# Optimization experiments

Measured on AMD Instinct MI355X. Metric: run time of the kernel, lower is better.

The kernel has to match this reference:

```python
import jax, jax.numpy as jnp
import numpy as np

D_MODEL = 1024
NHEAD = 16
HEAD_DIM = D_MODEL // NHEAD
DIM_FF = 4096
B, TC, TP = 4, 1024, 1024
EPS = 1e-5


def _layernorm(x, g, b):
    mu = jnp.mean(x, axis=-1, keepdims=True)
    var = jnp.mean(jnp.square(x - mu), axis=-1, keepdims=True)
    return (x - mu) * jax.lax.rsqrt(var + EPS) * g + b


def setup_inputs() -> dict:
    key = jax.random.key(0)
    ks = jax.random.split(key, 12)
    s = 0.02
    return {
        "x": jax.random.normal(ks[0], (B, TC, D_MODEL), jnp.float32),
        "Kp": jax.random.normal(ks[1], (B, NHEAD, TP, HEAD_DIM), jnp.float32),
        "Vp": jax.random.normal(ks[2], (B, NHEAD, TP, HEAD_DIM), jnp.float32),
        "pos_offset": TP,
        "wqkv": jax.random.normal(ks[3], (D_MODEL, 3 * D_MODEL), jnp.float32) * s,
        "bqkv": jnp.zeros((3 * D_MODEL,), jnp.float32),
        "wo": jax.random.normal(ks[4], (D_MODEL, D_MODEL), jnp.float32) * s,
        "bo": jnp.zeros((D_MODEL,), jnp.float32),
        "g1": jnp.ones((D_MODEL,), jnp.float32),
        "be1": jnp.zeros((D_MODEL,), jnp.float32),
        "g2": jnp.ones((D_MODEL,), jnp.float32),
        "be2": jnp.zeros((D_MODEL,), jnp.float32),
        "w1": jax.random.normal(ks[5], (D_MODEL, DIM_FF), jnp.float32) * s,
        "bf1": jnp.zeros((DIM_FF,), jnp.float32),
        "w2": jax.random.normal(ks[6], (DIM_FF, D_MODEL), jnp.float32) * s,
        "bf2": jnp.zeros((D_MODEL,), jnp.float32),
    }


def reference(x, Kp, Vp, pos_offset, wqkv, bqkv, wo, bo, g1, be1, g2, be2, w1, bf1, w2, bf2):
    Bsz, Tc, D = x.shape
    H, Dh = NHEAD, HEAD_DIM
    h = _layernorm(x, g1, be1)
    qkv = (h @ wqkv + bqkv).reshape(Bsz, Tc, 3, H, Dh).transpose(2, 0, 3, 1, 4)
    q, k_new, v_new = qkv[0], qkv[1], qkv[2]  # [B,H,Tc,Dh]
    K = jnp.concatenate([Kp, k_new], axis=2)  # [B,H,Tk,Dh]
    V = jnp.concatenate([Vp, v_new], axis=2)
    Tk = K.shape[2]
    scale = Dh ** -0.5
    # fused causal-masked attention; equivalent to the per-token loop:
    # query i attends keys j with j <= pos_offset + i
    scores = jnp.einsum("bhqd,bhkd->bhqk", q, K) * scale
    q_idx = jnp.arange(Tc)[:, None]
    k_idx = jnp.arange(Tk)[None, :]
    mask = k_idx <= (pos_offset + q_idx)  # [Tc,Tk]
    scores = jnp.where(mask, scores, jnp.finfo(scores.dtype).min)
    attn = jax.nn.softmax(scores, axis=-1)
    o = jnp.einsum("bhqk,bhkd->bhqd", attn, V)
    o = o.transpose(0, 2, 1, 3).reshape(Bsz, Tc, D)
    x = x + o @ wo + bo
    h2 = _layernorm(x, g2, be2)
    ff = jax.nn.gelu(h2 @ w1 + bf1, approximate=False) @ w2 + bf2
    x = x + ff
    return x, K, V
```

## Files before the change

### kernel.cpp

```cpp
#include <hip/hip_runtime.h>
#include <math.h>

#define DM   1024
#define NH   16
#define DH   64
#define DFF  4096
#define BSZ  4
#define TCC  1024
#define TPP  1024
#define TKK  2048
#define NTOK (BSZ*TCC)

typedef __attribute__((ext_vector_type(8))) short bf16x8;
typedef __attribute__((ext_vector_type(4))) float f32x4;

__device__ __forceinline__ unsigned short f2bf(float x) {
  union { float f; unsigned u; } v; v.f = x;
  unsigned r = v.u + 0x7fffu + ((v.u >> 16) & 1u);
  return (unsigned short)(r >> 16);
}
__device__ __forceinline__ unsigned pk2(float a, float b) {
  return (unsigned)f2bf(a) | ((unsigned)f2bf(b) << 16);
}

__device__ __forceinline__ void gload16(const void* g, void* l) {
  __builtin_amdgcn_global_load_lds(
      (const __attribute__((address_space(1))) void*)g,
      (__attribute__((address_space(3))) void*)l, 16, 0, 0);
}

__device__ __forceinline__ float wave_reduce_sum(float v) {
#pragma unroll
  for (int off = 32; off > 0; off >>= 1)
    v += __shfl_down(v, off, 64);
  return v;
}

__device__ __forceinline__ float gelu_f(float x) {
  return 0.5f * x * (1.0f + erff(x * 0.70710678118654752440f));
}

__global__ __launch_bounds__(256) void castT_kernel(
    const float* __restrict__ W, unsigned short* __restrict__ Wt, int K, int N) {
  __shared__ float tile[32][33];
  int nb = blockIdx.x << 5, kb = blockIdx.y << 5;
  int c = threadIdx.x & 31, r8 = threadIdx.x >> 5;
#pragma unroll
  for (int i = 0; i < 32; i += 8)
    tile[r8 + i][c] = W[(size_t)(kb + r8 + i) * N + nb + c];
  __syncthreads();
#pragma unroll
  for (int i = 0; i < 32; i += 8)
    Wt[(size_t)(nb + r8 + i) * K + kb + c] = f2bf(tile[c][r8 + i]);
}

__global__ __launch_bounds__(256) void castVt_kernel(
    const float* __restrict__ V, unsigned short* __restrict__ Vt) {
  __shared__ float tile[32][33];
  int z = blockIdx.z;
  const float* W = V + (size_t)z * TKK * DH;
  unsigned short* Wt = Vt + (size_t)z * DH * TKK;
  int nb = blockIdx.x << 5;
  int kb = blockIdx.y << 5;
  int c = threadIdx.x & 31, r8 = threadIdx.x >> 5;
#pragma unroll
  for (int i = 0; i < 32; i += 8)
    tile[r8 + i][c] = W[(size_t)(kb + r8 + i) * DH + nb + c];
  __syncthreads();
#pragma unroll
  for (int i = 0; i < 32; i += 8)
    Wt[(size_t)(nb + r8 + i) * TKK + kb + c] = f2bf(tile[c][r8 + i]);
}

__global__ __launch_bounds__(256) void copy_kv_kernel(
    const float4* __restrict__ Kp, const float4* __restrict__ Vp,
    float4* __restrict__ Kout, float4* __restrict__ Vout) {
  int idx = blockIdx.x * 256 + threadIdx.x;
  int r = idx >> 4;
  int c = idx & 15;
  int dr = (r >> 10) * TKK + (r & 1023);
  Kout[dr * 16 + c] = Kp[idx];
  Vout[dr * 16 + c] = Vp[idx];
}

__global__ __launch_bounds__(256) void ln_kernel(
    const float* __restrict__ x, const float* __restrict__ g,
    const float* __restrict__ b, unsigned short* __restrict__ out) {
  __shared__ float red[8];
  int row = blockIdx.x;
  int tid = threadIdx.x;
  const float4* xr = (const float4*)(x + (size_t)row * DM);
  float4 xv = xr[tid];
  float s  = xv.x + xv.y + xv.z + xv.w;
  float ss = xv.x*xv.x + xv.y*xv.y + xv.z*xv.z + xv.w*xv.w;
  s  = wave_reduce_sum(s);
  ss = wave_reduce_sum(ss);
  int lane = tid & 63, wid = tid >> 6;
  if (lane == 0) { red[wid] = s; red[4 + wid] = ss; }
  __syncthreads();
  s  = red[0] + red[1] + red[2] + red[3];
  ss = red[4] + red[5] + red[6] + red[7];
  float mu  = s * (1.0f / DM);
  float var = ss * (1.0f / DM) - mu * mu;
  float rs  = rsqrtf(var + 1e-5f);
  float4 gv = ((const float4*)g)[tid];
  float4 bv = ((const float4*)b)[tid];
  ushort4 ov;
  ov.x = f2bf((xv.x - mu) * rs * gv.x + bv.x);
  ov.y = f2bf((xv.y - mu) * rs * gv.y + bv.y);
  ov.z = f2bf((xv.z - mu) * rs * gv.z + bv.z);
  ov.w = f2bf((xv.w - mu) * rs * gv.w + bv.w);
  *(ushort4*)&out[(size_t)row * DM + tid * 4] = ov;
}

template <int MODE>
__global__ __launch_bounds__(256) void mm_kernel(
    const unsigned short* __restrict__ A, const unsigned short* __restrict__ Bt,
    const float* __restrict__ bias, const float* __restrict__ res,
    float* __restrict__ outf, unsigned short* __restrict__ outb,
    float* __restrict__ Kc, float* __restrict__ Vc,
    int M, int N, int K) {
  __shared__ __align__(16) short As[128 * 32];
  __shared__ __align__(16) short Bs[128 * 32];
  int tid = threadIdx.x;
  int w = tid >> 6, l = tid & 63;
  int m0 = blockIdx.y << 7, n0 = blockIdx.x << 7;
  int wm = (w >> 1) << 6, wn = (w & 1) << 6;
  int cidx = l & 15, rg = l >> 4;
  f32x4 acc[4][4] = {};

  int idx0 = w * 1024 + l * 16;
  int idx1 = idx0 + 4096;
  const char* gA0 = (const char*)A + (size_t)(m0 + (idx0 >> 6)) * 2 * K + (idx0 & 63);
  const char* gA1 = (const char*)A + (size_t)(m0 + (idx1 >> 6)) * 2 * K + (idx1 & 63);
  const char* gB0 = (const char*)Bt + (size_t)(n0 + (idx0 >> 6)) * 2 * K + (idx0 & 63);
  const char* gB1 = (const char*)Bt + (size_t)(n0 + (idx1 >> 6)) * 2 * K + (idx1 & 63);
  char* lA0 = (char*)As + idx0; char* lA1 = (char*)As + idx1;
  char* lB0 = (char*)Bs + idx0; char* lB1 = (char*)Bs + idx1;

  for (int k0 = 0; k0 < K; k0 += 32) {
    gload16(gA0, lA0); gload16(gA1, lA1);
    gload16(gB0, lB0); gload16(gB1, lB1);
    gA0 += 64; gA1 += 64; gB0 += 64; gB1 += 64;
    __syncthreads();
    bf16x8 af[4], bfr[4];
#pragma unroll
    for (int i = 0; i < 4; ++i) {
      af[i]  = *(const bf16x8*)&As[(wm + i * 16 + cidx) * 32 + rg * 8];
      bfr[i] = *(const bf16x8*)&Bs[(wn + i * 16 + cidx) * 32 + rg * 8];
    }
#pragma unroll
    for (int i = 0; i < 4; ++i)
#pragma unroll
      for (int j = 0; j < 4; ++j)
        acc[i][j] = __builtin_amdgcn_mfma_f32_16x16x32_bf16(
            af[i], bfr[j], acc[i][j], 0, 0, 0);
    __syncthreads();
  }

#pragma unroll
  for (int i = 0; i < 4; ++i) {
#pragma unroll
    for (int j = 0; j < 4; ++j) {
      int col = n0 + wn + j * 16 + cidx;
      float bb = bias[col];
#pragma unroll
      for (int r = 0; r < 4; ++r) {
        int row = m0 + wm + i * 16 + rg * 4 + r;
        float v = acc[i][j][r] + bb;
        if (MODE == 0) {
          int which = col >> 10, c = col & 1023;
          int hh = c >> 6, dd = c & 63;
          int b = row >> 10, t = row & 1023;
          size_t base = (size_t)(b * NH + hh);
          if (which == 0)      outb[(base * TCC + t) * DH + dd] = f2bf(v * 0.125f);
          else if (which == 1) Kc[(base * TKK + TPP + t) * DH + dd] = v;
          else                 Vc[(base * TKK + TPP + t) * DH + dd] = v;
        } else if (MODE == 1) {
          size_t off = (size_t)row * N + col;
          outf[off] = res[off] + v;
        } else {
          outb[(size_t)row * N + col] = f2bf(gelu_f(v));
        }
      }
    }
  }
}

__global__ __launch_bounds__(256) void attn_kernel(
    const unsigned short* __restrict__ Qb, const float* __restrict__ K,
    const unsigned short* __restrict__ Vtb, const int* __restrict__ posp,
    unsigned short* __restrict__ o) {
  __shared__ __align__(16) unsigned short Qs[64][72];
  __shared__ __align__(16) unsigned short Ks[64][72];
  __shared__ __align__(16) unsigned short Vts[64][72];
  __shared__ __align__(16) unsigned short Pw[4][16][72];
  int tid = threadIdx.x;
  int w = tid >> 6, lane = tid & 63;
  int l15 = lane & 15, quad = lane >> 4;
  int blk = blockIdx.x;
  int bh = blk >> 4;
  int qbase = (blk & 15) << 6;
  int b = bh >> 4, h = bh & 15;
  int pos = *posp;

  {
    int r = tid >> 2, cg = (tid & 3) << 4;
    const unsigned short* src = Qb + ((size_t)bh * TCC + qbase + r) * DH + cg;
    *(uint4*)&Qs[r][cg]     = *(const uint4*)src;
    *(uint4*)&Qs[r][cg + 8] = *(const uint4*)(src + 8);
  }
  __syncthreads();
  bf16x8 aq0 = *(const bf16x8*)&Qs[16 * w + l15][quad * 8];
  bf16x8 aq1 = *(const bf16x8*)&Qs[16 * w + l15][32 + quad * 8];

  f32x4 accO[4] = {};
  f32x4 accL = {};
  bf16x8 ones;
#pragma unroll
  for (int i = 0; i < 8; ++i) ones[i] = (short)0x3F80;

  int nk = pos + qbase + 64; if (nk > TKK) nk = TKK;
  int ntiles = nk >> 6;
  const float* Kbh = K + (size_t)bh * TKK * DH;
  const unsigned short* Vbh = Vtb + (size_t)bh * DH * TKK;

  for (int t = 0; t < ntiles; ++t) {
    int kt = t << 6;
    {
      int r = tid >> 2, cg = (tid & 3) << 4;
      const float* ks = Kbh + (size_t)(kt + r) * DH + cg;
      float4 k0 = *(const float4*)ks,       k1 = *(const float4*)(ks + 4);
      float4 k2 = *(const float4*)(ks + 8), k3 = *(const float4*)(ks + 12);
      uint4 p0, p1;
      p0.x = pk2(k0.x, k0.y); p0.y = pk2(k0.z, k0.w);
      p0.z = pk2(k1.x, k1.y); p0.w = pk2(k1.z, k1.w);
      p1.x = pk2(k2.x, k2.y); p1.y = pk2(k2.z, k2.w);
      p1.z = pk2(k3.x, k3.y); p1.w = pk2(k3.z, k3.w);
      *(uint4*)&Ks[r][cg]     = p0;
      *(uint4*)&Ks[r][cg + 8] = p1;
      const unsigned short* vs = Vbh + (size_t)r * TKK + kt + cg;
      *(uint4*)&Vts[r][cg]     = *(const uint4*)vs;
      *(uint4*)&Vts[r][cg + 8] = *(const uint4*)(vs + 8);
    }
    __syncthreads();
    f32x4 accS[4] = {};
#pragma unroll
    for (int j = 0; j < 4; ++j) {
      bf16x8 bk0 = *(const bf16x8*)&Ks[16 * j + l15][quad * 8];
      bf16x8 bk1 = *(const bf16x8*)&Ks[16 * j + l15][32 + quad * 8];
      accS[j] = __builtin_amdgcn_mfma_f32_16x16x32_bf16(aq0, bk0, accS[j], 0, 0, 0);
      accS[j] = __builtin_amdgcn_mfma_f32_16x16x32_bf16(aq1, bk1, accS[j], 0, 0, 0);
    }
    bool edge = (kt + 63 > pos + qbase);
#pragma unroll
    for (int j = 0; j < 4; ++j) {
      int key = kt + 16 * j + l15;
#pragma unroll
      for (int r = 0; r < 4; ++r) {
        float p = __expf(accS[j][r]);
        if (edge && key > pos + qbase + 16 * w + quad * 4 + r) p = 0.f;
        Pw[w][quad * 4 + r][16 * j + l15] = f2bf(p);
      }
    }
    bf16x8 ap0 = *(const bf16x8*)&Pw[w][l15][quad * 8];
    bf16x8 ap1 = *(const bf16x8*)&Pw[w][l15][32 + quad * 8];
    accL = __builtin_amdgcn_mfma_f32_16x16x32_bf16(ap0, ones, accL, 0, 0, 0);
    accL = __builtin_amdgcn_mfma_f32_16x16x32_bf16(ap1, ones, accL, 0, 0, 0);
#pragma unroll
    for (int j2 = 0; j2 < 4; ++j2) {
      bf16x8 bv0 = *(const bf16x8*)&Vts[16 * j2 + l15][quad * 8];
      bf16x8 bv1 = *(const bf16x8*)&Vts[16 * j2 + l15][32 + quad * 8];
      accO[j2] = __builtin_amdgcn_mfma_f32_16x16x32_bf16(ap0, bv0, accO[j2], 0, 0, 0);
      accO[j2] = __builtin_amdgcn_mfma_f32_16x16x32_bf16(ap1, bv1, accO[j2], 0, 0, 0);
    }
    __syncthreads();
  }
#pragma unroll
  for (int r = 0; r < 4; ++r) {
    float inv = 1.0f / accL[r];
    int qg = qbase + 16 * w + quad * 4 + r;
    size_t base = (((size_t)(b * TCC + qg)) * NH + h) * DH;
#pragma unroll
    for (int j2 = 0; j2 < 4; ++j2)
      o[base + 16 * j2 + l15] = f2bf(accO[j2][r] * inv);
  }
}

extern "C" void kernel_launch(void* const* d_in, const int* in_sizes, int n_in,
                              void* d_out, int out_size, void* d_ws, size_t ws_size,
                              hipStream_t stream) {
  (void)in_sizes; (void)n_in; (void)out_size; (void)ws_size;
  const float* x    = (const float*)d_in[0];
  const float* Kp   = (const float*)d_in[1];
  const float* Vp   = (const float*)d_in[2];
  const int*   posp = (const int*)d_in[3];
  const float* wqkv = (const float*)d_in[4];
  const float* bqkv = (const float*)d_in[5];
  const float* wo   = (const float*)d_in[6];
  const float* bo   = (const float*)d_in[7];
  const float* g1   = (const float*)d_in[8];
  const float* be1  = (const float*)d_in[9];
  const float* g2   = (const float*)d_in[10];
  const float* be2  = (const float*)d_in[11];
  const float* w1   = (const float*)d_in[12];
  const float* bf1  = (const float*)d_in[13];
  const float* w2   = (const float*)d_in[14];
  const float* bf2  = (const float*)d_in[15];

  float* xout = (float*)d_out;
  float* Kout = xout + (size_t)BSZ * TCC * DM;
  float* Vout = Kout + (size_t)BSZ * NH * TKK * DH;

  const size_t MB = 1024 * 1024;
  char* ws = (char*)d_ws;
  unsigned short* wqkvT = (unsigned short*)(ws);
  unsigned short* woT   = (unsigned short*)(ws + 6 * MB);
  unsigned short* w1T   = (unsigned short*)(ws + 8 * MB);
  unsigned short* w2T   = (unsigned short*)(ws + 16 * MB);
  unsigned short* hbf   = (unsigned short*)(ws + 24 * MB);
  unsigned short* ffbf  = (unsigned short*)(ws + 32 * MB);
  unsigned short* Qbuf  = (unsigned short*)(ws + 32 * MB);
  unsigned short* obf   = (unsigned short*)(ws + 40 * MB);
  unsigned short* Vtb   = (unsigned short*)(ws + 48 * MB);
  float*          x2    = xout;

  castT_kernel<<<dim3(96, 32),  dim3(256), 0, stream>>>(wqkv, wqkvT, DM, 3 * DM);
  castT_kernel<<<dim3(32, 32),  dim3(256), 0, stream>>>(wo,   woT,   DM, DM);
  castT_kernel<<<dim3(128, 32), dim3(256), 0, stream>>>(w1,   w1T,   DM, DFF);
  castT_kernel<<<dim3(32, 128), dim3(256), 0, stream>>>(w2,   w2T,   DFF, DM);

  copy_kv_kernel<<<dim3(4096), dim3(256), 0, stream>>>(
      (const float4*)Kp, (const float4*)Vp, (float4*)Kout, (float4*)Vout);
  ln_kernel<<<dim3(NTOK), dim3(256), 0, stream>>>(x, g1, be1, hbf);
  mm_kernel<0><<<dim3(24, 32), dim3(256), 0, stream>>>(
      hbf, wqkvT, bqkv, nullptr, nullptr, Qbuf, Kout, Vout, NTOK, 3 * DM, DM);
  castVt_kernel<<<dim3(2, 64, 64), dim3(256), 0, stream>>>(Vout, Vtb);
  attn_kernel<<<dim3(1024), dim3(256), 0, stream>>>(Qbuf, Kout, Vtb, posp, obf);
  mm_kernel<1><<<dim3(8, 32), dim3(256), 0, stream>>>(
      obf, woT, bo, x, x2, nullptr, nullptr, nullptr, NTOK, DM, DM);
  ln_kernel<<<dim3(NTOK), dim3(256), 0, stream>>>(x2, g2, be2, hbf);
  mm_kernel<2><<<dim3(32, 32), dim3(256), 0, stream>>>(
      hbf, w1T, bf1, nullptr, nullptr, ffbf, nullptr, nullptr, NTOK, DFF, DM);
  mm_kernel<1><<<dim3(8, 32), dim3(256), 0, stream>>>(
      ffbf, w2T, bf2, x2, xout, nullptr, nullptr, nullptr, NTOK, DM, DFF);
}
```

Measured before the change: 524.7 us.

## Precompute bf16 K copy, approximate erf in GELU, raise MFMA wave priority

Writes a bf16 copy of K during the KV copy and QKV projection epilogue, so attention loads half the bytes and skips per-tile conversion. This applies only when the workspace is at least 80 MB; otherwise the old path runs. It also swaps erff in GELU for the Abramowitz-Stegun polynomial with __expf, and wraps the attention MFMA blocks in s_setprio. The costs are extra bf16 stores upstream and slightly lower GELU accuracy.

```diff
diff --git a/kernel.cpp b/kernel.cpp
--- a/kernel.cpp
+++ b/kernel.cpp
@@ -37,7 +37,17 @@
 }
 
 __device__ __forceinline__ float gelu_f(float x) {
-  return 0.5f * x * (1.0f + erff(x * 0.70710678118654752440f));
+  float z = fabsf(x) * 0.70710678118654752440f;
+  float t = 1.0f / (1.0f + 0.3275911f * z);
+  float y = t * (0.254829592f +
+            t * (-0.284496736f +
+            t * (1.421413741f +
+            t * (-1.453152027f +
+            t * 1.061405429f))));
+  float e = __expf(-z * z);
+  float erfz = 1.0f - y * e;
+  float s = (x >= 0.0f) ? erfz : -erfz;
+  return 0.5f * x * (1.0f + s);
 }
 
 __global__ __launch_bounds__(256) void castT_kernel(
@@ -74,13 +84,21 @@
 
 __global__ __launch_bounds__(256) void copy_kv_kernel(
     const float4* __restrict__ Kp, const float4* __restrict__ Vp,
-    float4* __restrict__ Kout, float4* __restrict__ Vout) {
+    float4* __restrict__ Kout, float4* __restrict__ Vout,
+    unsigned short* __restrict__ Kbf) {
   int idx = blockIdx.x * 256 + threadIdx.x;
   int r = idx >> 4;
   int c = idx & 15;
   int dr = (r >> 10) * TKK + (r & 1023);
-  Kout[dr * 16 + c] = Kp[idx];
+  float4 kv = Kp[idx];
+  Kout[dr * 16 + c] = kv;
   Vout[dr * 16 + c] = Vp[idx];
+  if (Kbf != nullptr) {
+    uint2 pk;
+    pk.x = pk2(kv.x, kv.y);
+    pk.y = pk2(kv.z, kv.w);
+    *(uint2*)(Kbf + (size_t)(dr * 16 + c) * 4) = pk;
+  }
 }
 
 __global__ __launch_bounds__(256) void ln_kernel(
@@ -119,6 +137,7 @@
     const float* __restrict__ bias, const float* __restrict__ res,
     float* __restrict__ outf, unsigned short* __restrict__ outb,
     float* __restrict__ Kc, float* __restrict__ Vc,
+    unsigned short* __restrict__ Kbfp,
     int M, int N, int K) {
   __shared__ __align__(16) short As[128 * 32];
   __shared__ __align__(16) short Bs[128 * 32];
@@ -174,8 +193,11 @@
           int b = row >> 10, t = row & 1023;
           size_t base = (size_t)(b * NH + hh);
           if (which == 0)      outb[(base * TCC + t) * DH + dd] = f2bf(v * 0.125f);
-          else if (which == 1) Kc[(base * TKK + TPP + t) * DH + dd] = v;
-          else                 Vc[(base * TKK + TPP + t) * DH + dd] = v;
+          else if (which == 1) {
+            size_t off = (base * TKK + TPP + t) * DH + dd;
+            Kc[off] = v;
+            if (Kbfp != nullptr) Kbfp[off] = f2bf(v);
+          } else               Vc[(base * TKK + TPP + t) * DH + dd] = v;
         } else if (MODE == 1) {
           size_t off = (size_t)row * N + col;
           outf[off] = res[off] + v;
@@ -187,8 +209,10 @@
   }
 }
 
+template <int KBF>
 __global__ __launch_bounds__(256) void attn_kernel(
     const unsigned short* __restrict__ Qb, const float* __restrict__ K,
+    const unsigned short* __restrict__ Kb16,
     const unsigned short* __restrict__ Vtb, const int* __restrict__ posp,
     unsigned short* __restrict__ o) {
   __shared__ __align__(16) unsigned short Qs[64][72];
@@ -223,28 +247,36 @@
   int nk = pos + qbase + 64; if (nk > TKK) nk = TKK;
   int ntiles = nk >> 6;
   const float* Kbh = K + (size_t)bh * TKK * DH;
+  const unsigned short* Kbh16 = Kb16 + (size_t)bh * TKK * DH;
   const unsigned short* Vbh = Vtb + (size_t)bh * DH * TKK;
 
   for (int t = 0; t < ntiles; ++t) {
     int kt = t << 6;
     {
       int r = tid >> 2, cg = (tid & 3) << 4;
-      const float* ks = Kbh + (size_t)(kt + r) * DH + cg;
-      float4 k0 = *(const float4*)ks,       k1 = *(const float4*)(ks + 4);
-      float4 k2 = *(const float4*)(ks + 8), k3 = *(const float4*)(ks + 12);
-      uint4 p0, p1;
-      p0.x = pk2(k0.x, k0.y); p0.y = pk2(k0.z, k0.w);
-      p0.z = pk2(k1.x, k1.y); p0.w = pk2(k1.z, k1.w);
-      p1.x = pk2(k2.x, k2.y); p1.y = pk2(k2.z, k2.w);
-      p1.z = pk2(k3.x, k3.y); p1.w = pk2(k3.z, k3.w);
-      *(uint4*)&Ks[r][cg]     = p0;
-      *(uint4*)&Ks[r][cg + 8] = p1;
+      if (KBF) {
+        const unsigned short* ks = Kbh16 + (size_t)(kt + r) * DH + cg;
+        *(uint4*)&Ks[r][cg]     = *(const uint4*)ks;
+        *(uint4*)&Ks[r][cg + 8] = *(const uint4*)(ks + 8);
+      } else {
+        const float* ks = Kbh + (size_t)(kt + r) * DH + cg;
+        float4 k0 = *(const float4*)ks,       k1 = *(const float4*)(ks + 4);
+        float4 k2 = *(const float4*)(ks + 8), k3 = *(const float4*)(ks + 12);
+        uint4 p0, p1;
+        p0.x = pk2(k0.x, k0.y); p0.y = pk2(k0.z, k0.w);
+        p0.z = pk2(k1.x, k1.y); p0.w = pk2(k1.z, k1.w);
+        p1.x = pk2(k2.x, k2.y); p1.y = pk2(k2.z, k2.w);
+        p1.z = pk2(k3.x, k3.y); p1.w = pk2(k3.z, k3.w);
+        *(uint4*)&Ks[r][cg]     = p0;
+        *(uint4*)&Ks[r][cg + 8] = p1;
+      }
       const unsigned short* vs = Vbh + (size_t)r * TKK + kt + cg;
       *(uint4*)&Vts[r][cg]     = *(const uint4*)vs;
       *(uint4*)&Vts[r][cg + 8] = *(const uint4*)(vs + 8);
     }
     __syncthreads();
     f32x4 accS[4] = {};
+    __builtin_amdgcn_s_setprio(1);
 #pragma unroll
     for (int j = 0; j < 4; ++j) {
       bf16x8 bk0 = *(const bf16x8*)&Ks[16 * j + l15][quad * 8];
@@ -252,6 +284,7 @@
       accS[j] = __builtin_amdgcn_mfma_f32_16x16x32_bf16(aq0, bk0, accS[j], 0, 0, 0);
       accS[j] = __builtin_amdgcn_mfma_f32_16x16x32_bf16(aq1, bk1, accS[j], 0, 0, 0);
     }
+    __builtin_amdgcn_s_setprio(0);
     bool edge = (kt + 63 > pos + qbase);
 #pragma unroll
     for (int j = 0; j < 4; ++j) {
@@ -265,6 +298,7 @@
     }
     bf16x8 ap0 = *(const bf16x8*)&Pw[w][l15][quad * 8];
     bf16x8 ap1 = *(const bf16x8*)&Pw[w][l15][32 + quad * 8];
+    __builtin_amdgcn_s_setprio(1);
     accL = __builtin_amdgcn_mfma_f32_16x16x32_bf16(ap0, ones, accL, 0, 0, 0);
     accL = __builtin_amdgcn_mfma_f32_16x16x32_bf16(ap1, ones, accL, 0, 0, 0);
 #pragma unroll
@@ -274,6 +308,7 @@
       accO[j2] = __builtin_amdgcn_mfma_f32_16x16x32_bf16(ap0, bv0, accO[j2], 0, 0, 0);
       accO[j2] = __builtin_amdgcn_mfma_f32_16x16x32_bf16(ap1, bv1, accO[j2], 0, 0, 0);
     }
+    __builtin_amdgcn_s_setprio(0);
     __syncthreads();
   }
 #pragma unroll
@@ -290,7 +325,7 @@
 extern "C" void kernel_launch(void* const* d_in, const int* in_sizes, int n_in,
                               void* d_out, int out_size, void* d_ws, size_t ws_size,
                               hipStream_t stream) {
-  (void)in_sizes; (void)n_in; (void)out_size; (void)ws_size;
+  (void)in_sizes; (void)n_in; (void)out_size;
   const float* x    = (const float*)d_in[0];
   const float* Kp   = (const float*)d_in[1];
   const float* Vp   = (const float*)d_in[2];
@@ -324,6 +359,8 @@
   unsigned short* obf   = (unsigned short*)(ws + 40 * MB);
   unsigned short* Vtb   = (unsigned short*)(ws + 48 * MB);
   float*          x2    = xout;
+  unsigned short* Kbf   = (ws_size >= 80 * MB)
+                            ? (unsigned short*)(ws + 64 * MB) : nullptr;
 
   castT_kernel<<<dim3(96, 32),  dim3(256), 0, stream>>>(wqkv, wqkvT, DM, 3 * DM);
   castT_kernel<<<dim3(32, 32),  dim3(256), 0, stream>>>(wo,   woT,   DM, DM);
@@ -331,17 +368,20 @@
   castT_kernel<<<dim3(32, 128), dim3(256), 0, stream>>>(w2,   w2T,   DFF, DM);
 
   copy_kv_kernel<<<dim3(4096), dim3(256), 0, stream>>>(
-      (const float4*)Kp, (const float4*)Vp, (float4*)Kout, (float4*)Vout);
+      (const float4*)Kp, (const float4*)Vp, (float4*)Kout, (float4*)Vout, Kbf);
   ln_kernel<<<dim3(NTOK), dim3(256), 0, stream>>>(x, g1, be1, hbf);
   mm_kernel<0><<<dim3(24, 32), dim3(256), 0, stream>>>(
-      hbf, wqkvT, bqkv, nullptr, nullptr, Qbuf, Kout, Vout, NTOK, 3 * DM, DM);
+      hbf, wqkvT, bqkv, nullptr, nullptr, Qbuf, Kout, Vout, Kbf, NTOK, 3 * DM, DM);
   castVt_kernel<<<dim3(2, 64, 64), dim3(256), 0, stream>>>(Vout, Vtb);
-  attn_kernel<<<dim3(1024), dim3(256), 0, stream>>>(Qbuf, Kout, Vtb, posp, obf);
+  if (Kbf != nullptr)
+    attn_kernel<1><<<dim3(1024), dim3(256), 0, stream>>>(Qbuf, Kout, Kbf, Vtb, posp, obf);
+  else
+    attn_kernel<0><<<dim3(1024), dim3(256), 0, stream>>>(Qbuf, Kout, Kbf, Vtb, posp, obf);
   mm_kernel<1><<<dim3(8, 32), dim3(256), 0, stream>>>(
-      obf, woT, bo, x, x2, nullptr, nullptr, nullptr, NTOK, DM, DM);
+      obf, woT, bo, x, x2, nullptr, nullptr, nullptr, nullptr, NTOK, DM, DM);
   ln_kernel<<<dim3(NTOK), dim3(256), 0, stream>>>(x2, g2, be2, hbf);
   mm_kernel<2><<<dim3(32, 32), dim3(256), 0, stream>>>(
-      hbf, w1T, bf1, nullptr, nullptr, ffbf, nullptr, nullptr, NTOK, DFF, DM);
+      hbf, w1T, bf1, nullptr, nullptr, ffbf, nullptr, nullptr, nullptr, NTOK, DFF, DM);
   mm_kernel<1><<<dim3(8, 32), dim3(256), 0, stream>>>(
-      ffbf, w2T, bf2, x2, xout, nullptr, nullptr, nullptr, NTOK, DM, DFF);
-}
+      ffbf, w2T, bf2, x2, xout, nullptr, nullptr, nullptr, nullptr, NTOK, DM, DFF);
+}
```

Measured after the change: 508.2 us. 1.03x faster.
